# Kernel tuning notes

Hardware: AMD Instinct MI355X
Metric: run time of the kernel (lower is better)

The kernel has to match this reference:

```python
import jax, jax.numpy as jnp
import numpy as np

NUM_CODES = 512
CODE_DIM = 64
COMMITMENT_COST = 0.25


def setup_inputs() -> dict:
    key = jax.random.key(0)
    k1, k2 = jax.random.split(key)
    latents = jax.random.normal(k1, (32, 64, 64, CODE_DIM), dtype=jnp.float32)
    # torch init: uniform(-1/num_codes, 1/num_codes)
    codebook = jax.random.uniform(
        k2, (NUM_CODES, CODE_DIM), dtype=jnp.float32,
        minval=-1.0 / NUM_CODES, maxval=1.0 / NUM_CODES)
    return {"latents": latents, "codebook": codebook}


def reference(latents, codebook):
    shape = latents.shape
    flat = latents.reshape(-1, CODE_DIM)  # [N, D]
    # argmin of squared distance == argmin of cdist(p=2) distance.
    x2 = jnp.sum(flat * flat, axis=-1, keepdims=True)           # [N, 1]
    c2 = jnp.sum(codebook * codebook, axis=-1)                   # [K]
    d2 = x2 - 2.0 * (flat @ codebook.T) + c2[None, :]            # [N, K]
    codes_flat = jnp.argmin(d2, axis=-1)                         # [N] int
    codes = codes_flat.reshape(shape[:-1])

    quantized = codebook[codes_flat].reshape(shape)              # gather

    commitment = jnp.mean(jnp.square(latents - jax.lax.stop_gradient(quantized)))
    codebook_loss = jnp.mean(jnp.square(quantized - jax.lax.stop_gradient(latents)))

    # straight-through estimator
    quantized_st = latents + jax.lax.stop_gradient(quantized - latents)

    # perplexity histogram
    counts = jnp.bincount(codes_flat, length=NUM_CODES).astype(jnp.float32)
    probs = counts / jnp.sum(counts)
    entropy = -jnp.sum(probs * jnp.log(probs + 1e-10))
    perplexity = jnp.exp(entropy)

    return (quantized_st, codes,
            commitment * COMMITMENT_COST, codebook_loss, perplexity)
```

## Files before the change

### kernel.cpp

```cpp
#include <hip/hip_runtime.h>
#include <math.h>

#define N_ROWS 131072
#define DIMS 64
#define K_CODES 512
#define XS_STRIDE 68
#define NBLK 2048

typedef __attribute__((ext_vector_type(8))) short bf16x8;
typedef __attribute__((ext_vector_type(4))) float f32x4;

union B8 { uint4 u; bf16x8 h; };

__device__ inline unsigned bpack(float a, float b) {
  unsigned ua = __float_as_uint(a), ub = __float_as_uint(b);
  ua = (ua + 0x7FFFu + ((ua >> 16) & 1u)) >> 16;
  ub = (ub + 0x7FFFu + ((ub >> 16) & 1u)) >> 16;
  return ua | (ub << 16);
}

__device__ inline float exact_dot(const float* __restrict__ xr, const float* __restrict__ cr) {
  float m = 0.f;
  #pragma unroll
  for (int d4 = 0; d4 < 16; ++d4) {
    const float4 c = *(const float4*)&cr[d4 * 4];
    const float4 x = *(const float4*)&xr[d4 * 4];
    m = fmaf(x.x, c.x, m);
    m = fmaf(x.y, c.y, m);
    m = fmaf(x.z, c.z, m);
    m = fmaf(x.w, c.w, m);
  }
  return m;
}

__global__ __launch_bounds__(256) void vq_init(const float* __restrict__ codebook,
                                               int* __restrict__ bins,
                                               float* __restrict__ c2g,
                                               uint4* __restrict__ cbB) {
  #pragma clang fp contract(off)
  const int t = threadIdx.x;
  const int b = blockIdx.x;
  if (t < 64) {
    const int e = b * 64 + t;
    const int ct = e >> 7;
    const int q = e & 127;
    const int lane_id = q >> 1;
    const int half = q & 1;
    const int code = ct * 16 + (lane_id & 15);
    const int dbase = ((lane_id >> 4) * 8) + half * 32;
    const float* src = codebook + code * DIMS + dbase;
    const float4 a = *(const float4*)&src[0];
    const float4 c = *(const float4*)&src[4];
    uint4 u;
    u.x = bpack(a.x, a.y);
    u.y = bpack(a.z, a.w);
    u.z = bpack(c.x, c.y);
    u.w = bpack(c.z, c.w);
    cbB[e] = u;
  } else if (t < 72) {
    const int k = b * 8 + (t - 64);
    const float* cr = codebook + k * DIMS;
    float r[8];
    #pragma unroll
    for (int j = 0; j < 8; ++j) r[j] = cr[j] * cr[j];
    for (int i = 8; i < 64; i += 8) {
      #pragma unroll
      for (int j = 0; j < 8; ++j) r[j] += cr[i + j] * cr[i + j];
    }
    c2g[k] = ((r[0] + r[1]) + (r[2] + r[3])) + ((r[4] + r[5]) + (r[6] + r[7]));
  } else if (t < 80) {
    bins[b * 8 + (t - 72)] = 0;
  }
}

__global__ __launch_bounds__(256, 4) void vq_main(const float* __restrict__ latents,
                                                  const float* __restrict__ codebook,
                                                  const uint4* __restrict__ cbB,
                                                  const float* __restrict__ c2g,
                                                  float* __restrict__ out_st,
                                                  float* __restrict__ out_codes,
                                                  int* __restrict__ bins,
                                                  double* __restrict__ loss_part) {
  #pragma clang fp contract(off)
  __shared__ __align__(16) float xs[64 * XS_STRIDE];
  __shared__ float x2s[64];
  __shared__ float c2s[K_CODES];
  __shared__ float wmaxs[4];
  __shared__ float thr[64];
  __shared__ float pmin[4][64];
  __shared__ int cand_cnt[64];
  __shared__ int cand_k[64][16];
  __shared__ int rowk[64];
  __shared__ float pvv[4][64];
  __shared__ int pkk[4][64];
  __shared__ int ovf_rows[64];
  __shared__ int ovf_cnt;
  __shared__ double wsum[4];

  const int t = threadIdx.x;
  const int lane = t & 63;
  const int w = t >> 6;
  const int m = lane & 15;
  const int kq = lane >> 4;
  const int row0 = blockIdx.x * 64;

  {
    const float4* src = (const float4*)(latents + (size_t)row0 * DIMS);
    #pragma unroll
    for (int p = 0; p < 4; ++p) {
      const int f = p * 256 + t;
      *(float4*)&xs[(f >> 4) * XS_STRIDE + (f & 15) * 4] = src[f];
    }
    c2s[t] = c2g[t];
    c2s[t + 256] = c2g[t + 256];
    if (t < 64) cand_cnt[t] = 0;
    if (t == 0) ovf_cnt = 0;
  }
  __syncthreads();

  if (t < 64) {
    const float* xr = xs + t * XS_STRIDE;
    float r[8];
    #pragma unroll
    for (int j = 0; j < 8; ++j) r[j] = xr[j] * xr[j];
    #pragma unroll
    for (int i = 8; i < 64; i += 8) {
      #pragma unroll
      for (int j = 0; j < 8; ++j) r[j] += xr[i + j] * xr[i + j];
    }
    x2s[t] = ((r[0] + r[1]) + (r[2] + r[3])) + ((r[4] + r[5]) + (r[6] + r[7]));
  }
  {
    float mm = fmaxf(c2s[t], c2s[t + 256]);
    #pragma unroll
    for (int off = 1; off < 64; off <<= 1) mm = fmaxf(mm, __shfl_xor(mm, off));
    if (lane == 0) wmaxs[w] = mm;
  }
  __syncthreads();

  bf16x8 af0[4], af1[4];
  #pragma unroll
  for (int T = 0; T < 4; ++T) {
    const float* xr = xs + (T * 16 + m) * XS_STRIDE + kq * 8;
    const float4 a0 = *(const float4*)&xr[0];
    const float4 a1 = *(const float4*)&xr[4];
    const float4 b0 = *(const float4*)&xr[32];
    const float4 b1 = *(const float4*)&xr[36];
    B8 pa, pb;
    pa.u.x = bpack(a0.x, a0.y); pa.u.y = bpack(a0.z, a0.w);
    pa.u.z = bpack(a1.x, a1.y); pa.u.w = bpack(a1.z, a1.w);
    pb.u.x = bpack(b0.x, b0.y); pb.u.y = bpack(b0.z, b0.w);
    pb.u.z = bpack(b1.x, b1.y); pb.u.w = bpack(b1.z, b1.w);
    af0[T] = pa.h;
    af1[T] = pb.h;
  }

  float x2r[4][4];
  #pragma unroll
  for (int T = 0; T < 4; ++T)
    #pragma unroll
    for (int j = 0; j < 4; ++j) x2r[T][j] = x2s[T * 16 + kq * 4 + j];
  const int ct0 = w * 8;

  float mv[4][4];
  #pragma unroll
  for (int T = 0; T < 4; ++T)
    #pragma unroll
    for (int j = 0; j < 4; ++j) mv[T][j] = __builtin_inff();

  B8 cb0, cb1, nb0, nb1;
  cb0.u = cbB[ct0 * 128 + lane * 2 + 0];
  cb1.u = cbB[ct0 * 128 + lane * 2 + 1];
  #pragma unroll 1
  for (int q = 0; q < 8; ++q) {
    const int ct = ct0 + q;
    if (q < 7) {
      nb0.u = cbB[(ct + 1) * 128 + lane * 2 + 0];
      nb1.u = cbB[(ct + 1) * 128 + lane * 2 + 1];
    }
    const float c2v = c2s[ct * 16 + m];
    #pragma unroll
    for (int T = 0; T < 4; ++T) {
      f32x4 acc = {0.f, 0.f, 0.f, 0.f};
      acc = __builtin_amdgcn_mfma_f32_16x16x32_bf16(af0[T], cb0.h, acc, 0, 0, 0);
      acc = __builtin_amdgcn_mfma_f32_16x16x32_bf16(af1[T], cb1.h, acc, 0, 0, 0);
      #pragma unroll
      for (int j = 0; j < 4; ++j) {
        const float s = (x2r[T][j] - 2.0f * acc[j]) + c2v;
        mv[T][j] = fminf(mv[T][j], s);
      }
    }
    cb0 = nb0;
    cb1 = nb1;
  }
  #pragma unroll
  for (int T = 0; T < 4; ++T)
    #pragma unroll
    for (int j = 0; j < 4; ++j) {
      float v = mv[T][j];
      #pragma unroll
      for (int off = 1; off < 16; off <<= 1) v = fminf(v, __shfl_xor(v, off));
      mv[T][j] = v;
    }
  if (m == 0) {
    #pragma unroll
    for (int T = 0; T < 4; ++T)
      #pragma unroll
      for (int j = 0; j < 4; ++j) pmin[w][T * 16 + kq * 4 + j] = mv[T][j];
  }
  __syncthreads();
  if (t < 64) {
    const float gmin = fminf(fminf(pmin[0][t], pmin[1][t]), fminf(pmin[2][t], pmin[3][t]));
    const float cmax = sqrtf(fmaxf(fmaxf(wmaxs[0], wmaxs[1]), fmaxf(wmaxs[2], wmaxs[3]))) * 1.0001f;
    thr[t] = gmin + (sqrtf(x2s[t]) * cmax * 0.0427f + 1e-3f);
  }
  __syncthreads();

  float thrr[4][4];
  #pragma unroll
  for (int T = 0; T < 4; ++T)
    #pragma unroll
    for (int j = 0; j < 4; ++j) thrr[T][j] = thr[T * 16 + kq * 4 + j];

  cb0.u = cbB[ct0 * 128 + lane * 2 + 0];
  cb1.u = cbB[ct0 * 128 + lane * 2 + 1];
  #pragma unroll 1
  for (int q = 0; q < 8; ++q) {
    const int ct = ct0 + q;
    if (q < 7) {
      nb0.u = cbB[(ct + 1) * 128 + lane * 2 + 0];
      nb1.u = cbB[(ct + 1) * 128 + lane * 2 + 1];
    }
    const float c2v = c2s[ct * 16 + m];
    const int k = ct * 16 + m;
    #pragma unroll
    for (int T = 0; T < 4; ++T) {
      f32x4 acc = {0.f, 0.f, 0.f, 0.f};
      acc = __builtin_amdgcn_mfma_f32_16x16x32_bf16(af0[T], cb0.h, acc, 0, 0, 0);
      acc = __builtin_amdgcn_mfma_f32_16x16x32_bf16(af1[T], cb1.h, acc, 0, 0, 0);
      #pragma unroll
      for (int j = 0; j < 4; ++j) {
        const float s = (x2r[T][j] - 2.0f * acc[j]) + c2v;
        if (s <= thrr[T][j]) {
          const int rr = T * 16 + kq * 4 + j;
          const int pos = atomicAdd(&cand_cnt[rr], 1);
          if (pos < 16) cand_k[rr][pos] = k;
        }
      }
    }
    cb0 = nb0;
    cb1 = nb1;
  }
  __syncthreads();

  {
    const int rr = t & 63;
    const int ph = t >> 6;
    const int cnt = cand_cnt[rr];
    float bv = __builtin_inff();
    int bk = 0x7fffffff;
    if (cnt <= 16) {
      const float* xr = xs + rr * XS_STRIDE;
      const float x2e = x2s[rr];
      for (int c = ph; c < cnt; c += 4) {
        const int k = cand_k[rr][c];
        const float M = exact_dot(xr, codebook + k * DIMS);
        const float s = (x2e - 2.0f * M) + c2s[k];
        if (s < bv || (s == bv && k < bk)) { bv = s; bk = k; }
      }
    } else if (ph == 0) {
      const int p = atomicAdd(&ovf_cnt, 1);
      ovf_rows[p] = rr;
    }
    pvv[ph][rr] = bv;
    pkk[ph][rr] = bk;
  }
  __syncthreads();
  if (t < 64) {
    float bv = pvv[0][t];
    int bk = pkk[0][t];
    #pragma unroll
    for (int ph = 1; ph < 4; ++ph) {
      const float v = pvv[ph][t];
      const int k = pkk[ph][t];
      if (v < bv || (v == bv && k < bk)) { bv = v; bk = k; }
    }
    rowk[t] = bk;
  }
  __syncthreads();

  if (w == 0) {
    const int no = ovf_cnt;
    for (int o = 0; o < no; ++o) {
      const int rr = ovf_rows[o];
      const float* xr = xs + rr * XS_STRIDE;
      const float x2e = x2s[rr];
      float bv = __builtin_inff();
      int bk = 0x7fffffff;
      for (int k = lane; k < K_CODES; k += 64) {
        const float M = exact_dot(xr, codebook + k * DIMS);
        const float s = (x2e - 2.0f * M) + c2s[k];
        if (s < bv || (s == bv && k < bk)) { bv = s; bk = k; }
      }
      #pragma unroll
      for (int off = 1; off < 64; off <<= 1) {
        const float ov = __shfl_xor(bv, off);
        const int oi = __shfl_xor(bk, off);
        if (ov < bv || (ov == bv && oi < bk)) { bv = ov; bk = oi; }
      }
      if (lane == 0) rowk[rr] = bk;
    }
  }
  __syncthreads();

  if (t < 64) {
    const int k = rowk[t];
    out_codes[row0 + t] = (float)k;
    atomicAdd(&bins[k], 1);
  }
  double dacc = 0.0;
  {
    float4* dst = (float4*)out_st + (size_t)row0 * 16;
    #pragma unroll
    for (int p = 0; p < 4; ++p) {
      const int f = p * 256 + t;
      const int r = f >> 4;
      const int d4 = f & 15;
      const int k = rowk[r];
      const float4 q = *(const float4*)&codebook[k * DIMS + d4 * 4];
      const float4 l = *(const float4*)&xs[r * XS_STRIDE + d4 * 4];
      float4 o;
      o.x = l.x + (q.x - l.x);
      o.y = l.y + (q.y - l.y);
      o.z = l.z + (q.z - l.z);
      o.w = l.w + (q.w - l.w);
      dst[f] = o;
      const float dx = l.x - q.x, dy = l.y - q.y, dz = l.z - q.z, dw = l.w - q.w;
      dacc += (double)dx * (double)dx;
      dacc += (double)dy * (double)dy;
      dacc += (double)dz * (double)dz;
      dacc += (double)dw * (double)dw;
    }
  }
  #pragma unroll
  for (int off = 32; off > 0; off >>= 1) dacc += __shfl_down(dacc, off);
  if (lane == 0) wsum[w] = dacc;
  __syncthreads();
  if (t == 0) loss_part[blockIdx.x] = (wsum[0] + wsum[1]) + (wsum[2] + wsum[3]);
}

__global__ __launch_bounds__(512) void vq_finalize(const int* __restrict__ bins,
                                                   const double* __restrict__ loss_part,
                                                   float* __restrict__ out3) {
  __shared__ double red[512];
  __shared__ double redl[512];
  const int t = threadIdx.x;
  const double p = (double)bins[t] / 131072.0;
  red[t] = -p * log(p + 1e-10);
  redl[t] = (loss_part[t] + loss_part[t + 512]) + (loss_part[t + 1024] + loss_part[t + 1536]);
  __syncthreads();
  for (int s = 256; s > 0; s >>= 1) {
    if (t < s) { red[t] += red[t + s]; redl[t] += redl[t + s]; }
    __syncthreads();
  }
  if (t == 0) {
    const double mean = redl[0] / 8388608.0;
    out3[0] = (float)(0.25 * mean);
    out3[1] = (float)mean;
    out3[2] = (float)exp(red[0]);
  }
}

extern "C" void kernel_launch(void* const* d_in, const int* in_sizes, int n_in,
                              void* d_out, int out_size, void* d_ws, size_t ws_size,
                              hipStream_t stream) {
  const float* latents = (const float*)d_in[0];
  const float* codebook = (const float*)d_in[1];

  float* out = (float*)d_out;
  float* out_st = out;
  float* out_codes = out + (size_t)N_ROWS * DIMS;
  float* out3 = out_codes + N_ROWS;

  char* ws = (char*)d_ws;
  double* loss_part = (double*)ws;
  int* bins = (int*)(ws + 16384);
  float* c2g = (float*)(ws + 18432);
  uint4* cbB = (uint4*)(ws + 21504);

  hipLaunchKernelGGL(vq_init, dim3(64), dim3(256), 0, stream,
                     codebook, bins, c2g, cbB);
  hipLaunchKernelGGL(vq_main, dim3(NBLK), dim3(256), 0, stream,
                     latents, codebook, cbB, c2g, out_st, out_codes, bins, loss_part);
  hipLaunchKernelGGL(vq_finalize, dim3(1), dim3(512), 0, stream,
                     bins, loss_part, out3);
}
```

Before: 148.0 us.

## Fuse the two codebook MFMA passes into one pass tracking per-lane top-2

Previously the kernel ran the bf16 MFMA distance sweep over the codebook twice: once for the row minimum and once to collect candidates under a threshold. Now a single sweep keeps each lane's best and second-best partial distance (c2 minus twice the dot product, with x2 dropped) plus the best index. After the threshold is known, each lane's best is emitted as a candidate. If a lane's second-best also falls under the threshold, the candidate count is pushed past the limit so the row takes the exhaustive fallback path. This halves the MFMA and codebook-load work, but the absolute threshold margin is widened from 1e-3 to 4e-3, so more rows may hit the slower fallback.

```diff
diff --git a/kernel.cpp b/kernel.cpp
--- a/kernel.cpp
+++ b/kernel.cpp
@@ -155,18 +155,18 @@
     af1[T] = pb.h;
   }
 
-  float x2r[4][4];
+  const int ct0 = w * 8;
+
+  float u1[4][4], u2[4][4];
+  int k1[4][4];
   #pragma unroll
   for (int T = 0; T < 4; ++T)
     #pragma unroll
-    for (int j = 0; j < 4; ++j) x2r[T][j] = x2s[T * 16 + kq * 4 + j];
-  const int ct0 = w * 8;
-
-  float mv[4][4];
-  #pragma unroll
-  for (int T = 0; T < 4; ++T)
-    #pragma unroll
-    for (int j = 0; j < 4; ++j) mv[T][j] = __builtin_inff();
+    for (int j = 0; j < 4; ++j) {
+      u1[T][j] = __builtin_inff();
+      u2[T][j] = __builtin_inff();
+      k1[T][j] = 0x7fffffff;
+    }
 
   B8 cb0, cb1, nb0, nb1;
   cb0.u = cbB[ct0 * 128 + lane * 2 + 0];
@@ -179,6 +179,7 @@
       nb1.u = cbB[(ct + 1) * 128 + lane * 2 + 1];
     }
     const float c2v = c2s[ct * 16 + m];
+    const int kcur = ct * 16 + m;
     #pragma unroll
     for (int T = 0; T < 4; ++T) {
       f32x4 acc = {0.f, 0.f, 0.f, 0.f};
@@ -186,8 +187,11 @@
       acc = __builtin_amdgcn_mfma_f32_16x16x32_bf16(af1[T], cb1.h, acc, 0, 0, 0);
       #pragma unroll
       for (int j = 0; j < 4; ++j) {
-        const float s = (x2r[T][j] - 2.0f * acc[j]) + c2v;
-        mv[T][j] = fminf(mv[T][j], s);
+        const float u = c2v - 2.0f * acc[j];
+        const bool c = u < u1[T][j];
+        u2[T][j] = c ? u1[T][j] : fminf(u2[T][j], u);
+        k1[T][j] = c ? kcur : k1[T][j];
+        u1[T][j] = c ? u : u1[T][j];
       }
     }
     cb0 = nb0;
@@ -197,60 +201,31 @@
   for (int T = 0; T < 4; ++T)
     #pragma unroll
     for (int j = 0; j < 4; ++j) {
-      float v = mv[T][j];
+      float v = u1[T][j];
       #pragma unroll
       for (int off = 1; off < 16; off <<= 1) v = fminf(v, __shfl_xor(v, off));
-      mv[T][j] = v;
-    }
-  if (m == 0) {
-    #pragma unroll
-    for (int T = 0; T < 4; ++T)
-      #pragma unroll
-      for (int j = 0; j < 4; ++j) pmin[w][T * 16 + kq * 4 + j] = mv[T][j];
-  }
+      if (m == 0) pmin[w][T * 16 + kq * 4 + j] = v;
+    }
   __syncthreads();
   if (t < 64) {
     const float gmin = fminf(fminf(pmin[0][t], pmin[1][t]), fminf(pmin[2][t], pmin[3][t]));
     const float cmax = sqrtf(fmaxf(fmaxf(wmaxs[0], wmaxs[1]), fmaxf(wmaxs[2], wmaxs[3]))) * 1.0001f;
-    thr[t] = gmin + (sqrtf(x2s[t]) * cmax * 0.0427f + 1e-3f);
-  }
-  __syncthreads();
-
-  float thrr[4][4];
+    thr[t] = gmin + (sqrtf(x2s[t]) * cmax * 0.0427f + 4e-3f);
+  }
+  __syncthreads();
+
   #pragma unroll
   for (int T = 0; T < 4; ++T)
     #pragma unroll
-    for (int j = 0; j < 4; ++j) thrr[T][j] = thr[T * 16 + kq * 4 + j];
-
-  cb0.u = cbB[ct0 * 128 + lane * 2 + 0];
-  cb1.u = cbB[ct0 * 128 + lane * 2 + 1];
-  #pragma unroll 1
-  for (int q = 0; q < 8; ++q) {
-    const int ct = ct0 + q;
-    if (q < 7) {
-      nb0.u = cbB[(ct + 1) * 128 + lane * 2 + 0];
-      nb1.u = cbB[(ct + 1) * 128 + lane * 2 + 1];
-    }
-    const float c2v = c2s[ct * 16 + m];
-    const int k = ct * 16 + m;
-    #pragma unroll
-    for (int T = 0; T < 4; ++T) {
-      f32x4 acc = {0.f, 0.f, 0.f, 0.f};
-      acc = __builtin_amdgcn_mfma_f32_16x16x32_bf16(af0[T], cb0.h, acc, 0, 0, 0);
-      acc = __builtin_amdgcn_mfma_f32_16x16x32_bf16(af1[T], cb1.h, acc, 0, 0, 0);
-      #pragma unroll
-      for (int j = 0; j < 4; ++j) {
-        const float s = (x2r[T][j] - 2.0f * acc[j]) + c2v;
-        if (s <= thrr[T][j]) {
-          const int rr = T * 16 + kq * 4 + j;
-          const int pos = atomicAdd(&cand_cnt[rr], 1);
-          if (pos < 16) cand_k[rr][pos] = k;
-        }
-      }
-    }
-    cb0 = nb0;
-    cb1 = nb1;
-  }
+    for (int j = 0; j < 4; ++j) {
+      const int rr = T * 16 + kq * 4 + j;
+      const float th = thr[rr];
+      if (u1[T][j] <= th) {
+        const int pos = atomicAdd(&cand_cnt[rr], 1);
+        if (pos < 16) cand_k[rr][pos] = k1[T][j];
+      }
+      if (u2[T][j] <= th) atomicAdd(&cand_cnt[rr], 64);
+    }
   __syncthreads();
 
   {
```

Result: slower. 342.5 us (+131.4%).
